# Kernel optimization log

Hardware: AMD Instinct MI355X
Metric: run time of the kernel (lower is better)

The kernel has to match this reference:

```python
import jax, jax.numpy as jnp
import numpy as np

HEADS = 8
DIM_HEAD = 64
RMS_EPS = 1.1920929e-07  # torch default eps = finfo(fp32).eps


def rotate_half(x):
    x1, x2 = jnp.split(x, 2, axis=-1)
    return jnp.concatenate((-x2, x1), axis=-1)


def setup_inputs() -> dict:
    key = jax.random.key(0)
    k1, k2, k3, k4, k5 = jax.random.split(key, 5)
    b, n, dim = 2, 4096, 1024
    dim_hidden = HEADS * DIM_HEAD  # 512
    x = jax.random.normal(k1, (b, n, dim), dtype=jnp.float32)
    rotary_emb = jax.random.normal(k2, (n, DIM_HEAD), dtype=jnp.float32)
    rms_weight = jnp.ones((dim,), dtype=jnp.float32)
    w_qkv = jax.random.normal(k3, (dim, dim_hidden * 3), dtype=jnp.float32) * (dim ** -0.5)
    w_out = jax.random.normal(k4, (dim_hidden, dim), dtype=jnp.float32) * (dim_hidden ** -0.5)
    return {"x": x, "rotary_emb": rotary_emb, "rms_weight": rms_weight,
            "w_qkv": w_qkv, "w_out": w_out}


def reference(x, rotary_emb, rms_weight, w_qkv, w_out):
    b, n, dim = x.shape
    h, d = HEADS, DIM_HEAD
    # RMSNorm
    xn = x * jax.lax.rsqrt(jnp.mean(x * x, axis=-1, keepdims=True) + RMS_EPS) * rms_weight
    # QKV projection, rearrange 'b n (qkv h d) -> qkv b h n d'
    qkv = (xn @ w_qkv).reshape(b, n, 3, h, d).transpose(2, 0, 3, 1, 4)
    q, k, v = qkv[0], qkv[1], qkv[2]
    # RoPE
    cos, sin = jnp.cos(rotary_emb), jnp.sin(rotary_emb)  # (n, d) broadcasts over b,h
    q = q * cos + rotate_half(q) * sin
    k = k * cos + rotate_half(k) * sin
    q = q * (d ** -0.5)
    sim = jnp.einsum('bhid,bhjd->bhij', q, k)
    causal_mask = jnp.triu(jnp.ones((n, n), dtype=bool), 1)
    sim = jnp.where(causal_mask, -jnp.finfo(sim.dtype).max, sim)
    attn = jax.nn.softmax(sim, axis=-1)
    out = jnp.einsum('bhij,bhjd->bhid', attn, v)
    out = out.transpose(0, 2, 1, 3).reshape(b, n, h * d)  # 'b h n d -> b n (h d)'
    return out @ w_out
```

## Files before the change

### kernel.cpp

```cpp
#include <hip/hip_runtime.h>
#include <hip/hip_bf16.h>
#include <cstdint>

using bf16x8 = __attribute__((ext_vector_type(8))) __bf16;
using f32x4  = __attribute__((ext_vector_type(4))) float;

#define LOG2E 1.4426950408889634f

__device__ inline void gload16(__bf16* lds, const __bf16* g) {
    __builtin_amdgcn_global_load_lds((const __attribute__((address_space(1))) void*)g,
                                     (__attribute__((address_space(3))) void*)lds, 16, 0, 0);
}
__device__ inline void wait_barrier4() {
    asm volatile("s_waitcnt vmcnt(4)" ::: "memory");
    __builtin_amdgcn_s_barrier();
}
__device__ inline void wait_barrier0() {
    asm volatile("s_waitcnt vmcnt(0)" ::: "memory");
    __builtin_amdgcn_s_barrier();
}

__global__ __launch_bounds__(256) void rmsnorm_kernel(const float* __restrict__ x,
                                                      const float* __restrict__ w,
                                                      __bf16* __restrict__ xn) {
    const int row = blockIdx.x;
    const float4 v = reinterpret_cast<const float4*>(x + (size_t)row * 1024)[threadIdx.x];
    float ss = v.x * v.x + v.y * v.y + v.z * v.z + v.w * v.w;
#pragma unroll
    for (int i = 1; i < 64; i <<= 1) ss += __shfl_xor(ss, i);
    __shared__ float part[4];
    if ((threadIdx.x & 63) == 0) part[threadIdx.x >> 6] = ss;
    __syncthreads();
    const float total = part[0] + part[1] + part[2] + part[3];
    const float scale = rsqrtf(total * (1.0f / 1024.0f) + 1.1920929e-07f);
    const float4 wv = reinterpret_cast<const float4*>(w)[threadIdx.x];
    union { __bf16 h[4]; uint2 u; } pk;
    pk.h[0] = (__bf16)(v.x * scale * wv.x);
    pk.h[1] = (__bf16)(v.y * scale * wv.y);
    pk.h[2] = (__bf16)(v.z * scale * wv.z);
    pk.h[3] = (__bf16)(v.w * scale * wv.w);
    reinterpret_cast<uint2*>(xn + (size_t)row * 1024)[threadIdx.x] = pk.u;
}

__global__ void transpose_cast_kernel(const float* __restrict__ in,
                                      __bf16* __restrict__ out, int K, int N) {
    __shared__ float tile[32][33];
    const int n0 = blockIdx.x * 32, k0 = blockIdx.y * 32;
#pragma unroll
    for (int r = threadIdx.y; r < 32; r += 8)
        tile[r][threadIdx.x] = in[(size_t)(k0 + r) * N + n0 + threadIdx.x];
    __syncthreads();
#pragma unroll
    for (int r = threadIdx.y; r < 32; r += 8)
        out[(size_t)(n0 + r) * K + k0 + threadIdx.x] = (__bf16)tile[threadIdx.x][r];
}

__global__ __launch_bounds__(256) void csin_kernel(const float* __restrict__ rot,
                                                   float2* __restrict__ csin) {
    const int i = blockIdx.x * 256 + threadIdx.x;
    float s, c;
    sincosf(rot[i], &s, &c);
    csin[i] = make_float2(c, s);
}

__global__ __launch_bounds__(256) void rope_kernel(__bf16* __restrict__ qk,
                                                   const float2* __restrict__ csin) {
    const int row = blockIdx.x * 4 + (threadIdx.x >> 6);
    const int lane = threadIdx.x & 63;
    const int h = lane >> 3, dl = (lane & 7) * 4;
    const int pos = row & 4095;
    const float4 csA = *reinterpret_cast<const float4*>(&csin[pos * 64 + dl]);
    const float4 csB = *reinterpret_cast<const float4*>(&csin[pos * 64 + dl + 2]);
    const float4 csC = *reinterpret_cast<const float4*>(&csin[pos * 64 + dl + 32]);
    const float4 csD = *reinterpret_cast<const float4*>(&csin[pos * 64 + dl + 34]);
    const float c0[4] = {csA.x, csA.z, csB.x, csB.z};
    const float s0[4] = {csA.y, csA.w, csB.y, csB.w};
    const float c1[4] = {csC.x, csC.z, csD.x, csD.z};
    const float s1[4] = {csC.y, csC.w, csD.y, csD.w};
    __bf16* p = qk + (size_t)row * 1024 + h * 64 + dl;
    const float qs = 0.125f * LOG2E;
#pragma unroll
    for (int part = 0; part < 2; ++part) {
        __bf16* pp = p + part * 512;
        const float sc = part ? 1.0f : qs;
        union { uint2 u; __bf16 hh[4]; } va, vb, oa, ob;
        va.u = *reinterpret_cast<const uint2*>(pp);
        vb.u = *reinterpret_cast<const uint2*>(pp + 32);
#pragma unroll
        for (int j = 0; j < 4; ++j) {
            const float a = (float)va.hh[j], b2 = (float)vb.hh[j];
            oa.hh[j] = (__bf16)((a * c0[j] - b2 * s0[j]) * sc);
            ob.hh[j] = (__bf16)((b2 * c1[j] + a * s1[j]) * sc);
        }
        *reinterpret_cast<uint2*>(pp)      = oa.u;
        *reinterpret_cast<uint2*>(pp + 32) = ob.u;
    }
}

template <typename OutT, int MODE>
__global__ __launch_bounds__(256) void gemm_bt(const __bf16* __restrict__ A,
                                               const __bf16* __restrict__ Bt,
                                               OutT* __restrict__ C,
                                               __bf16* __restrict__ vt,
                                               int M, int N, int K) {
    __shared__ __align__(16) __bf16 As[3][128 * 32];
    __shared__ __align__(16) __bf16 Bs[3][128 * 32];
    const int bm = blockIdx.y, bn = blockIdx.x;
    const int tid = threadIdx.x;
    const int w = tid >> 6, l = tid & 63, lg = l >> 4, lr = l & 15;
    const int wr = w >> 1, wc = w & 1;
    const __bf16* Ab = A + (size_t)(bm * 128) * K;
    const __bf16* Bb = Bt + (size_t)(bn * 128) * K;
    const int srow = tid >> 2, scol = (tid & 3) * 8;
    const __bf16* Asrc = Ab + (size_t)srow * K + scol;
    const __bf16* Bsrc = Bb + (size_t)srow * K + scol;

    auto stage = [&](int k2) {
        const int nx = k2 % 3;
        const int off = k2 * 32;
        gload16(&As[nx][tid * 8],        Asrc + off);
        gload16(&As[nx][2048 + tid * 8], Asrc + (size_t)64 * K + off);
        gload16(&Bs[nx][tid * 8],        Bsrc + off);
        gload16(&Bs[nx][2048 + tid * 8], Bsrc + (size_t)64 * K + off);
    };

    const int NS = K >> 5;
    f32x4 acc[4][4] = {};
    stage(0);
    stage(1);
    wait_barrier4();
    for (int k = 0; k < NS; ++k) {
        const bool more = (k + 2 < NS);
        if (more) stage(k + 2);
        const __bf16* Ac = &As[k % 3][0];
        const __bf16* Bc = &Bs[k % 3][0];
        bf16x8 af[4], bfr[4];
#pragma unroll
        for (int m = 0; m < 4; ++m)
            af[m] = *reinterpret_cast<const bf16x8*>(Ac + (wr * 64 + m * 16 + lr) * 32 + lg * 8);
#pragma unroll
        for (int nn = 0; nn < 4; ++nn)
            bfr[nn] = *reinterpret_cast<const bf16x8*>(Bc + (wc * 64 + nn * 16 + lr) * 32 + lg * 8);
#pragma unroll
        for (int m = 0; m < 4; ++m)
#pragma unroll
            for (int nn = 0; nn < 4; ++nn)
                acc[m][nn] = __builtin_amdgcn_mfma_f32_16x16x32_bf16(af[m], bfr[nn],
                                                                     acc[m][nn], 0, 0, 0);
        if (more) wait_barrier4();
        else      wait_barrier0();
    }
    if constexpr (MODE == 1) {
        const int cb = bn * 128 + wc * 64;
        if (cb < 1024) {
#pragma unroll
            for (int m = 0; m < 4; ++m) {
                const int rg = bm * 128 + wr * 64 + m * 16 + 4 * lg;
#pragma unroll
                for (int nn = 0; nn < 4; ++nn) {
                    const int cg = cb + nn * 16 + lr;
#pragma unroll
                    for (int r = 0; r < 4; ++r)
                        C[(size_t)(rg + r) * 1024 + cg] = (OutT)acc[m][nn][r];
                }
            }
        } else {
#pragma unroll
            for (int m = 0; m < 4; ++m) {
                const int rg = bm * 128 + wr * 64 + m * 16 + 4 * lg;
                const int bidx = rg >> 12, pos0 = rg & 4095;
                const int a0 = pos0 & 63;
                const int cp = 32 * (a0 >> 5) + 8 * ((a0 >> 2) & 3) + 4 * ((a0 >> 4) & 1);
                const int nbase = (pos0 & ~63) + cp;
#pragma unroll
                for (int nn = 0; nn < 4; ++nn) {
                    const int col = cb + nn * 16 + lr - 1024;
                    const int hh = col >> 6, dd = col & 63;
                    union { __bf16 h4[4]; uint2 u; } pk2;
#pragma unroll
                    for (int r = 0; r < 4; ++r) pk2.h4[r] = (__bf16)acc[m][nn][r];
                    *reinterpret_cast<uint2*>(&vt[((size_t)(bidx * 8 + hh) * 64 + dd) * 4096 + nbase]) = pk2.u;
                }
            }
        }
        return;
    }
#pragma unroll
    for (int m = 0; m < 4; ++m) {
        const int rg = bm * 128 + wr * 64 + m * 16 + 4 * lg;
#pragma unroll
        for (int nn = 0; nn < 4; ++nn) {
            const int cg = bn * 128 + wc * 64 + nn * 16 + lr;
#pragma unroll
            for (int r = 0; r < 4; ++r)
                C[(size_t)(rg + r) * N + cg] = (OutT)acc[m][nn][r];
        }
    }
}

__global__ __launch_bounds__(256) void attn_kernel(const __bf16* __restrict__ qkp,
                                                   const __bf16* __restrict__ vt,
                                                   __bf16* __restrict__ attn_out) {
    const int bid = blockIdx.x;
    const int swz = (bid & 7) * 64 + (bid >> 3);
    const int bh  = swz >> 5;
    const int p   = swz & 31;
    const int b = bh >> 3, h = bh & 7;
    const int tid = threadIdx.x;
    const int w = tid >> 6, l = tid & 63, lg = l >> 4, lr = l & 15;

    __shared__ __align__(16) __bf16 Ks[4][64 * 64];
    __shared__ __align__(16) __bf16 Vs[4][64 * 64];

    const __bf16* qbase = qkp + (size_t)b * 4096 * 1024 + h * 64;
    const __bf16* kbase = qbase + 512;
    const __bf16* vtb   = vt + (size_t)(b * 8 + h) * 64 * 4096;

    const int sr = tid >> 3;
    const int sc = ((tid & 7) ^ (sr & 7)) * 8;
    const __bf16* ksrc0 = kbase + (size_t)sr * 1024 + sc;
    const __bf16* vsrc0 = vtb + (size_t)sr * 4096 + sc;

    const int xel = (lr & 7) * 8;

    for (int seg = 0; seg < 2; ++seg) {
        const int qt = seg ? (63 - p) : p;
        const int wq0 = qt * 64 + 16 * w;
        const int nkt = qt + 1;

        bf16x8 Qf[2];
#pragma unroll
        for (int kh = 0; kh < 2; ++kh)
            Qf[kh] = *reinterpret_cast<const bf16x8*>(
                qbase + (size_t)(wq0 + lr) * 1024 + 32 * kh + 8 * lg);

        f32x4 O[4] = {};
        float m_ = -1e30f, l_ = 0.0f;
        const __bf16* kp = ksrc0;
        const __bf16* vp = vsrc0;

        auto stage2 = [&](__bf16* kdst, __bf16* vdst) {
            gload16(kdst + tid * 8,         kp);
            gload16(kdst + (tid + 256) * 8, kp + 32 * 1024);
            gload16(vdst + tid * 8,         vp);
            gload16(vdst + (tid + 256) * 8, vp + 32 * 4096);
            kp += 64 * 1024;
            vp += 64;
        };
        auto qk_step = [&](f32x4 (&S)[4], const __bf16* kb) {
            __builtin_amdgcn_s_setprio(1);
#pragma unroll
            for (int jt = 0; jt < 4; ++jt) {
                const __bf16* kr = kb + (16 * jt + lr) * 64;
                const bf16x8 Kf0 = *reinterpret_cast<const bf16x8*>(kr + ((8 * lg) ^ xel));
                const bf16x8 Kf1 = *reinterpret_cast<const bf16x8*>(kr + ((32 + 8 * lg) ^ xel));
                f32x4 z = {};
                z = __builtin_amdgcn_mfma_f32_16x16x32_bf16(Kf0, Qf[0], z, 0, 0, 0);
                S[jt] = __builtin_amdgcn_mfma_f32_16x16x32_bf16(Kf1, Qf[1], z, 0, 0, 0);
            }
            __builtin_amdgcn_s_setprio(0);
        };
        auto smpv = [&](f32x4 (&SC)[4], const __bf16* vb, bool domask) {
            if (domask) {
#pragma unroll
                for (int jt = 0; jt < 4; ++jt)
#pragma unroll
                    for (int r = 0; r < 4; ++r)
                        if (16 * jt + 4 * lg + r > 16 * w + lr) SC[jt][r] = -1e30f;
            }
            float mx = -1e30f;
#pragma unroll
            for (int jt = 0; jt < 4; ++jt)
                mx = fmaxf(mx, fmaxf(fmaxf(SC[jt][0], SC[jt][1]), fmaxf(SC[jt][2], SC[jt][3])));
            if (__any(mx > m_ + 8.0f)) {
                mx = fmaxf(mx, __shfl_xor(mx, 16));
                mx = fmaxf(mx, __shfl_xor(mx, 32));
                const float mn = fmaxf(m_, mx);
                const float alpha = __builtin_amdgcn_exp2f(m_ - mn);
                m_ = mn;
                l_ *= alpha;
#pragma unroll
                for (int dt = 0; dt < 4; ++dt) O[dt] *= alpha;
            }
            float sum = 0.0f;
#pragma unroll
            for (int jt = 0; jt < 4; ++jt)
#pragma unroll
                for (int r = 0; r < 4; ++r) {
                    const float pv = __builtin_amdgcn_exp2f(SC[jt][r] - m_);
                    SC[jt][r] = pv;
                    sum += pv;
                }
            l_ += sum;
            __builtin_amdgcn_s_setprio(1);
#pragma unroll
            for (int s = 0; s < 2; ++s) {
                bf16x8 Pf;
#pragma unroll
                for (int i = 0; i < 8; ++i)
                    Pf[i] = (__bf16)SC[2 * s + (i >> 2)][i & 3];
#pragma unroll
                for (int dt = 0; dt < 4; ++dt) {
                    const bf16x8 Vf = *reinterpret_cast<const bf16x8*>(
                        vb + (16 * dt + lr) * 64 + ((32 * s + 8 * lg) ^ xel));
                    O[dt] = __builtin_amdgcn_mfma_f32_16x16x32_bf16(Vf, Pf, O[dt], 0, 0, 0);
                }
            }
            __builtin_amdgcn_s_setprio(0);
        };

        f32x4 S0[4], S1[4];
        int t = 0;

        stage2(Ks[0], Vs[0]);
        stage2(Ks[1], Vs[1]);
        stage2(Ks[2], Vs[2]);
        wait_barrier4();
        qk_step(S0, Ks[0]);

        for (; t + 8 <= nkt; t += 4) {
            stage2(Ks[3], Vs[3]); qk_step(S1, Ks[1]); smpv(S0, Vs[0], false); wait_barrier4();
            stage2(Ks[0], Vs[0]); qk_step(S0, Ks[2]); smpv(S1, Vs[1], false); wait_barrier4();
            stage2(Ks[1], Vs[1]); qk_step(S1, Ks[3]); smpv(S0, Vs[2], false); wait_barrier4();
            stage2(Ks[2], Vs[2]); qk_step(S0, Ks[0]); smpv(S1, Vs[3], false); wait_barrier4();
        }

        {
            f32x4 Sp[4];
#pragma unroll
            for (int jt = 0; jt < 4; ++jt) Sp[jt] = S0[jt];
            for (; t < nkt; ++t) {
                const bool more3 = (t + 3 < nkt);
                if (more3) stage2(Ks[(t + 3) & 3], Vs[(t + 3) & 3]);
                f32x4 Sn[4];
                if (t + 1 < nkt) qk_step(Sn, Ks[(t + 1) & 3]);
                smpv(Sp, Vs[t & 3], t == nkt - 1);
                if (more3) wait_barrier4();
                else       wait_barrier0();
#pragma unroll
                for (int jt = 0; jt < 4; ++jt) Sp[jt] = Sn[jt];
            }
        }

        float lt = l_;
        lt += __shfl_xor(lt, 16);
        lt += __shfl_xor(lt, 32);
        const float inv = 1.0f / lt;
        __bf16* op = attn_out + ((size_t)b * 4096 + wq0 + lr) * 512 + h * 64;
#pragma unroll
        for (int dt = 0; dt < 4; ++dt) {
            union { __bf16 h4[4]; uint2 u; } ow;
#pragma unroll
            for (int r = 0; r < 4; ++r) ow.h4[r] = (__bf16)(O[dt][r] * inv);
            *reinterpret_cast<uint2*>(op + 16 * dt + 4 * lg) = ow.u;
        }
    }
}

extern "C" void kernel_launch(void* const* d_in, const int* in_sizes, int n_in,
                              void* d_out, int out_size, void* d_ws, size_t ws_size,
                              hipStream_t stream) {
    (void)in_sizes; (void)n_in; (void)out_size; (void)ws_size;
    const float* x    = (const float*)d_in[0];
    const float* rot  = (const float*)d_in[1];
    const float* rmsw = (const float*)d_in[2];
    const float* wqkv = (const float*)d_in[3];
    const float* wout = (const float*)d_in[4];
    float* out = (float*)d_out;

    char* ws = (char*)d_ws;
    __bf16* xn    = (__bf16*)ws;
    __bf16* wqkvt = (__bf16*)(ws + 16777216);
    __bf16* woutt = (__bf16*)(ws + 16777216 + 3145728);
    __bf16* aout  = (__bf16*)(ws + 16777216 + 3145728 + 1048576);
    __bf16* qk   = (__bf16*)d_out;
    float2* csin = (float2*)((char*)d_out + 16777216);
    __bf16* vt   = (__bf16*)((char*)d_out + 18874368);

    rmsnorm_kernel<<<8192, 256, 0, stream>>>(x, rmsw, xn);
    transpose_cast_kernel<<<dim3(48, 32), dim3(32, 8), 0, stream>>>(wqkv, wqkvt, 1024, 1536);
    transpose_cast_kernel<<<dim3(32, 16), dim3(32, 8), 0, stream>>>(wout, woutt, 512, 1024);
    csin_kernel<<<1024, 256, 0, stream>>>(rot, csin);
    gemm_bt<__bf16, 1><<<dim3(12, 64), 256, 0, stream>>>(xn, wqkvt, qk, vt, 8192, 1536, 1024);
    rope_kernel<<<2048, 256, 0, stream>>>(qk, csin);
    attn_kernel<<<512, 256, 0, stream>>>(qk, vt, aout);
    gemm_bt<float, 0><<<dim3(8, 64), 256, 0, stream>>>(aout, woutt, out, nullptr, 8192, 1024, 512);
}
```

Measured before the change: 142.8 us.

## Split attention into one query tile per block, triple-buffer KV, stage GEMM epilogue via LDS

The attention kernel now launches 1024 blocks, each handling a single query tile. Tiles are ordered longest-first so the causal workload balances across CUs. This replaces the old scheme where each of 512 blocks processed a paired short and long tile. The KV ring buffer shrinks from 4 to 3 stages, which cuts LDS use so more blocks can be resident, but the waits become full __syncthreads drains instead of partial vmcnt waits. Separately, the GEMM epilogue stages accumulators through LDS so each row is written with wide coalesced 16-byte stores rather than scattered scalar stores.

```diff
diff --git a/kernel.cpp b/kernel.cpp
--- a/kernel.cpp
+++ b/kernel.cpp
@@ -150,21 +150,10 @@
         if (more) wait_barrier4();
         else      wait_barrier0();
     }
+
+    const int cb = bn * 128 + wc * 64;
     if constexpr (MODE == 1) {
-        const int cb = bn * 128 + wc * 64;
-        if (cb < 1024) {
-#pragma unroll
-            for (int m = 0; m < 4; ++m) {
-                const int rg = bm * 128 + wr * 64 + m * 16 + 4 * lg;
-#pragma unroll
-                for (int nn = 0; nn < 4; ++nn) {
-                    const int cg = cb + nn * 16 + lr;
-#pragma unroll
-                    for (int r = 0; r < 4; ++r)
-                        C[(size_t)(rg + r) * 1024 + cg] = (OutT)acc[m][nn][r];
-                }
-            }
-        } else {
+        if (cb >= 1024) {
 #pragma unroll
             for (int m = 0; m < 4; ++m) {
                 const int rg = bm * 128 + wr * 64 + m * 16 + 4 * lg;
@@ -182,18 +171,36 @@
                     *reinterpret_cast<uint2*>(&vt[((size_t)(bidx * 8 + hh) * 64 + dd) * 4096 + nbase]) = pk2.u;
                 }
             }
-        }
-        return;
-    }
+            return;
+        }
+    }
+    float* tb = reinterpret_cast<float*>(&As[0][0]) + w * 1088;
+    const int row = l >> 2, c4 = (l & 3) * 16;
 #pragma unroll
     for (int m = 0; m < 4; ++m) {
-        const int rg = bm * 128 + wr * 64 + m * 16 + 4 * lg;
-#pragma unroll
-        for (int nn = 0; nn < 4; ++nn) {
-            const int cg = bn * 128 + wc * 64 + nn * 16 + lr;
+#pragma unroll
+        for (int nn = 0; nn < 4; ++nn)
 #pragma unroll
             for (int r = 0; r < 4; ++r)
-                C[(size_t)(rg + r) * N + cg] = (OutT)acc[m][nn][r];
+                tb[(4 * lg + r) * 68 + nn * 16 + lr] = acc[m][nn][r];
+        const int rg2 = bm * 128 + wr * 64 + m * 16 + row;
+        float v[16];
+#pragma unroll
+        for (int j = 0; j < 4; ++j)
+            *reinterpret_cast<float4*>(v + 4 * j) =
+                *reinterpret_cast<const float4*>(tb + row * 68 + c4 + 4 * j);
+        if constexpr (MODE == 1) {
+            union { __bf16 h16[16]; uint4 u4[2]; } ob;
+#pragma unroll
+            for (int j = 0; j < 16; ++j) ob.h16[j] = (__bf16)v[j];
+            uint4* dst = reinterpret_cast<uint4*>(C + (size_t)rg2 * 1024 + cb + c4);
+            dst[0] = ob.u4[0];
+            dst[1] = ob.u4[1];
+        } else {
+#pragma unroll
+            for (int j = 0; j < 4; ++j)
+                *reinterpret_cast<float4*>(&C[(size_t)rg2 * N + cb + c4 + 4 * j]) =
+                    *reinterpret_cast<const float4*>(v + 4 * j);
         }
     }
 }
@@ -202,15 +209,15 @@
                                                    const __bf16* __restrict__ vt,
                                                    __bf16* __restrict__ attn_out) {
     const int bid = blockIdx.x;
-    const int swz = (bid & 7) * 64 + (bid >> 3);
-    const int bh  = swz >> 5;
-    const int p   = swz & 31;
+    const int j = bid >> 3;
+    const int bh = 2 * (bid & 7) + (j & 1);
+    const int qt = 63 - (j >> 1);
     const int b = bh >> 3, h = bh & 7;
     const int tid = threadIdx.x;
     const int w = tid >> 6, l = tid & 63, lg = l >> 4, lr = l & 15;
 
-    __shared__ __align__(16) __bf16 Ks[4][64 * 64];
-    __shared__ __align__(16) __bf16 Vs[4][64 * 64];
+    __shared__ __align__(16) __bf16 Ks[3][64 * 64];
+    __shared__ __align__(16) __bf16 Vs[3][64 * 64];
 
     const __bf16* qbase = qkp + (size_t)b * 4096 * 1024 + h * 64;
     const __bf16* kbase = qbase + 512;
@@ -218,142 +225,136 @@
 
     const int sr = tid >> 3;
     const int sc = ((tid & 7) ^ (sr & 7)) * 8;
-    const __bf16* ksrc0 = kbase + (size_t)sr * 1024 + sc;
-    const __bf16* vsrc0 = vtb + (size_t)sr * 4096 + sc;
+    const __bf16* kp = kbase + (size_t)sr * 1024 + sc;
+    const __bf16* vp = vtb + (size_t)sr * 4096 + sc;
 
     const int xel = (lr & 7) * 8;
 
-    for (int seg = 0; seg < 2; ++seg) {
-        const int qt = seg ? (63 - p) : p;
-        const int wq0 = qt * 64 + 16 * w;
-        const int nkt = qt + 1;
-
-        bf16x8 Qf[2];
-#pragma unroll
-        for (int kh = 0; kh < 2; ++kh)
-            Qf[kh] = *reinterpret_cast<const bf16x8*>(
-                qbase + (size_t)(wq0 + lr) * 1024 + 32 * kh + 8 * lg);
-
-        f32x4 O[4] = {};
-        float m_ = -1e30f, l_ = 0.0f;
-        const __bf16* kp = ksrc0;
-        const __bf16* vp = vsrc0;
-
-        auto stage2 = [&](__bf16* kdst, __bf16* vdst) {
-            gload16(kdst + tid * 8,         kp);
-            gload16(kdst + (tid + 256) * 8, kp + 32 * 1024);
-            gload16(vdst + tid * 8,         vp);
-            gload16(vdst + (tid + 256) * 8, vp + 32 * 4096);
-            kp += 64 * 1024;
-            vp += 64;
-        };
-        auto qk_step = [&](f32x4 (&S)[4], const __bf16* kb) {
-            __builtin_amdgcn_s_setprio(1);
-#pragma unroll
-            for (int jt = 0; jt < 4; ++jt) {
-                const __bf16* kr = kb + (16 * jt + lr) * 64;
-                const bf16x8 Kf0 = *reinterpret_cast<const bf16x8*>(kr + ((8 * lg) ^ xel));
-                const bf16x8 Kf1 = *reinterpret_cast<const bf16x8*>(kr + ((32 + 8 * lg) ^ xel));
-                f32x4 z = {};
-                z = __builtin_amdgcn_mfma_f32_16x16x32_bf16(Kf0, Qf[0], z, 0, 0, 0);
-                S[jt] = __builtin_amdgcn_mfma_f32_16x16x32_bf16(Kf1, Qf[1], z, 0, 0, 0);
+    const int wq0 = qt * 64 + 16 * w;
+    const int nkt = qt + 1;
+
+    bf16x8 Qf[2];
+#pragma unroll
+    for (int kh = 0; kh < 2; ++kh)
+        Qf[kh] = *reinterpret_cast<const bf16x8*>(
+            qbase + (size_t)(wq0 + lr) * 1024 + 32 * kh + 8 * lg);
+
+    f32x4 O[4] = {};
+    float m_ = -1e30f, l_ = 0.0f;
+
+    auto stage2 = [&](__bf16* kdst, __bf16* vdst) {
+        gload16(kdst + tid * 8,         kp);
+        gload16(kdst + (tid + 256) * 8, kp + 32 * 1024);
+        gload16(vdst + tid * 8,         vp);
+        gload16(vdst + (tid + 256) * 8, vp + 32 * 4096);
+        kp += 64 * 1024;
+        vp += 64;
+    };
+    auto qk_step = [&](f32x4 (&S)[4], const __bf16* kb) {
+        __builtin_amdgcn_s_setprio(1);
+#pragma unroll
+        for (int jt = 0; jt < 4; ++jt) {
+            const __bf16* kr = kb + (16 * jt + lr) * 64;
+            const bf16x8 Kf0 = *reinterpret_cast<const bf16x8*>(kr + ((8 * lg) ^ xel));
+            const bf16x8 Kf1 = *reinterpret_cast<const bf16x8*>(kr + ((32 + 8 * lg) ^ xel));
+            f32x4 z = {};
+            z = __builtin_amdgcn_mfma_f32_16x16x32_bf16(Kf0, Qf[0], z, 0, 0, 0);
+            S[jt] = __builtin_amdgcn_mfma_f32_16x16x32_bf16(Kf1, Qf[1], z, 0, 0, 0);
+        }
+        __builtin_amdgcn_s_setprio(0);
+    };
+    auto smpv = [&](f32x4 (&SC)[4], const __bf16* vb, bool domask) {
+        if (domask) {
+#pragma unroll
+            for (int jt = 0; jt < 4; ++jt)
+#pragma unroll
+                for (int r = 0; r < 4; ++r)
+                    if (16 * jt + 4 * lg + r > 16 * w + lr) SC[jt][r] = -1e30f;
+        }
+        float mx = -1e30f;
+#pragma unroll
+        for (int jt = 0; jt < 4; ++jt)
+            mx = fmaxf(mx, fmaxf(fmaxf(SC[jt][0], SC[jt][1]), fmaxf(SC[jt][2], SC[jt][3])));
+        if (__any(mx > m_ + 8.0f)) {
+            mx = fmaxf(mx, __shfl_xor(mx, 16));
+            mx = fmaxf(mx, __shfl_xor(mx, 32));
+            const float mn = fmaxf(m_, mx);
+            const float alpha = __builtin_amdgcn_exp2f(m_ - mn);
+            m_ = mn;
+            l_ *= alpha;
+#pragma unroll
+            for (int dt = 0; dt < 4; ++dt) O[dt] *= alpha;
+        }
+        float sum = 0.0f;
+#pragma unroll
+        for (int jt = 0; jt < 4; ++jt)
+#pragma unroll
+            for (int r = 0; r < 4; ++r) {
+                const float pv = __builtin_amdgcn_exp2f(SC[jt][r] - m_);
+                SC[jt][r] = pv;
+                sum += pv;
             }
-            __builtin_amdgcn_s_setprio(0);
-        };
-        auto smpv = [&](f32x4 (&SC)[4], const __bf16* vb, bool domask) {
-            if (domask) {
-#pragma unroll
-                for (int jt = 0; jt < 4; ++jt)
-#pragma unroll
-                    for (int r = 0; r < 4; ++r)
-                        if (16 * jt + 4 * lg + r > 16 * w + lr) SC[jt][r] = -1e30f;
+        l_ += sum;
+        __builtin_amdgcn_s_setprio(1);
+#pragma unroll
+        for (int s = 0; s < 2; ++s) {
+            bf16x8 Pf;
+#pragma unroll
+            for (int i = 0; i < 8; ++i)
+                Pf[i] = (__bf16)SC[2 * s + (i >> 2)][i & 3];
+#pragma unroll
+            for (int dt = 0; dt < 4; ++dt) {
+                const bf16x8 Vf = *reinterpret_cast<const bf16x8*>(
+                    vb + (16 * dt + lr) * 64 + ((32 * s + 8 * lg) ^ xel));
+                O[dt] = __builtin_amdgcn_mfma_f32_16x16x32_bf16(Vf, Pf, O[dt], 0, 0, 0);
             }
-            float mx = -1e30f;
-#pragma unroll
-            for (int jt = 0; jt < 4; ++jt)
-                mx = fmaxf(mx, fmaxf(fmaxf(SC[jt][0], SC[jt][1]), fmaxf(SC[jt][2], SC[jt][3])));
-            if (__any(mx > m_ + 8.0f)) {
-                mx = fmaxf(mx, __shfl_xor(mx, 16));
-                mx = fmaxf(mx, __shfl_xor(mx, 32));
-                const float mn = fmaxf(m_, mx);
-                const float alpha = __builtin_amdgcn_exp2f(m_ - mn);
-                m_ = mn;
-                l_ *= alpha;
-#pragma unroll
-                for (int dt = 0; dt < 4; ++dt) O[dt] *= alpha;
-            }
-            float sum = 0.0f;
-#pragma unroll
-            for (int jt = 0; jt < 4; ++jt)
-#pragma unroll
-                for (int r = 0; r < 4; ++r) {
-                    const float pv = __builtin_amdgcn_exp2f(SC[jt][r] - m_);
-                    SC[jt][r] = pv;
-                    sum += pv;
-                }
-            l_ += sum;
-            __builtin_amdgcn_s_setprio(1);
-#pragma unroll
-            for (int s = 0; s < 2; ++s) {
-                bf16x8 Pf;
-#pragma unroll
-                for (int i = 0; i < 8; ++i)
-                    Pf[i] = (__bf16)SC[2 * s + (i >> 2)][i & 3];
-#pragma unroll
-                for (int dt = 0; dt < 4; ++dt) {
-                    const bf16x8 Vf = *reinterpret_cast<const bf16x8*>(
-                        vb + (16 * dt + lr) * 64 + ((32 * s + 8 * lg) ^ xel));
-                    O[dt] = __builtin_amdgcn_mfma_f32_16x16x32_bf16(Vf, Pf, O[dt], 0, 0, 0);
-                }
-            }
-            __builtin_amdgcn_s_setprio(0);
-        };
-
-        f32x4 S0[4], S1[4];
-        int t = 0;
-
-        stage2(Ks[0], Vs[0]);
-        stage2(Ks[1], Vs[1]);
-        stage2(Ks[2], Vs[2]);
-        wait_barrier4();
-        qk_step(S0, Ks[0]);
-
-        for (; t + 8 <= nkt; t += 4) {
-            stage2(Ks[3], Vs[3]); qk_step(S1, Ks[1]); smpv(S0, Vs[0], false); wait_barrier4();
-            stage2(Ks[0], Vs[0]); qk_step(S0, Ks[2]); smpv(S1, Vs[1], false); wait_barrier4();
-            stage2(Ks[1], Vs[1]); qk_step(S1, Ks[3]); smpv(S0, Vs[2], false); wait_barrier4();
-            stage2(Ks[2], Vs[2]); qk_step(S0, Ks[0]); smpv(S1, Vs[3], false); wait_barrier4();
-        }
-
-        {
-            f32x4 Sp[4];
-#pragma unroll
-            for (int jt = 0; jt < 4; ++jt) Sp[jt] = S0[jt];
-            for (; t < nkt; ++t) {
-                const bool more3 = (t + 3 < nkt);
-                if (more3) stage2(Ks[(t + 3) & 3], Vs[(t + 3) & 3]);
-                f32x4 Sn[4];
-                if (t + 1 < nkt) qk_step(Sn, Ks[(t + 1) & 3]);
-                smpv(Sp, Vs[t & 3], t == nkt - 1);
-                if (more3) wait_barrier4();
-                else       wait_barrier0();
-#pragma unroll
-                for (int jt = 0; jt < 4; ++jt) Sp[jt] = Sn[jt];
-            }
-        }
-
-        float lt = l_;
-        lt += __shfl_xor(lt, 16);
-        lt += __shfl_xor(lt, 32);
-        const float inv = 1.0f / lt;
-        __bf16* op = attn_out + ((size_t)b * 4096 + wq0 + lr) * 512 + h * 64;
-#pragma unroll
-        for (int dt = 0; dt < 4; ++dt) {
-            union { __bf16 h4[4]; uint2 u; } ow;
-#pragma unroll
-            for (int r = 0; r < 4; ++r) ow.h4[r] = (__bf16)(O[dt][r] * inv);
-            *reinterpret_cast<uint2*>(op + 16 * dt + 4 * lg) = ow.u;
-        }
+        }
+        __builtin_amdgcn_s_setprio(0);
+    };
+
+    f32x4 S0[4], S1[4];
+    int t = 0;
+
+    stage2(Ks[0], Vs[0]);
+    stage2(Ks[1], Vs[1]);
+    __syncthreads();
+    qk_step(S0, Ks[0]);
+
+    for (; t + 8 <= nkt; t += 6) {
+        stage2(Ks[2], Vs[2]); qk_step(S1, Ks[1]); smpv(S0, Vs[0], false); __syncthreads();
+        stage2(Ks[0], Vs[0]); qk_step(S0, Ks[2]); smpv(S1, Vs[1], false); __syncthreads();
+        stage2(Ks[1], Vs[1]); qk_step(S1, Ks[0]); smpv(S0, Vs[2], false); __syncthreads();
+        stage2(Ks[2], Vs[2]); qk_step(S0, Ks[1]); smpv(S1, Vs[0], false); __syncthreads();
+        stage2(Ks[0], Vs[0]); qk_step(S1, Ks[2]); smpv(S0, Vs[1], false); __syncthreads();
+        stage2(Ks[1], Vs[1]); qk_step(S0, Ks[0]); smpv(S1, Vs[2], false); __syncthreads();
+    }
+
+    {
+        f32x4 Sp[4];
+#pragma unroll
+        for (int jt = 0; jt < 4; ++jt) Sp[jt] = S0[jt];
+        for (; t < nkt; ++t) {
+            if (t + 2 < nkt) stage2(Ks[(t + 2) % 3], Vs[(t + 2) % 3]);
+            f32x4 Sn[4];
+            if (t + 1 < nkt) qk_step(Sn, Ks[(t + 1) % 3]);
+            smpv(Sp, Vs[t % 3], t == nkt - 1);
+            __syncthreads();
+#pragma unroll
+            for (int jt = 0; jt < 4; ++jt) Sp[jt] = Sn[jt];
+        }
+    }
+
+    float lt = l_;
+    lt += __shfl_xor(lt, 16);
+    lt += __shfl_xor(lt, 32);
+    const float inv = 1.0f / lt;
+    __bf16* op = attn_out + ((size_t)b * 4096 + wq0 + lr) * 512 + h * 64;
+#pragma unroll
+    for (int dt = 0; dt < 4; ++dt) {
+        union { __bf16 h4[4]; uint2 u; } ow;
+#pragma unroll
+        for (int r = 0; r < 4; ++r) ow.h4[r] = (__bf16)(O[dt][r] * inv);
+        *reinterpret_cast<uint2*>(op + 16 * dt + 4 * lg) = ow.u;
     }
 }
 
@@ -383,6 +384,6 @@
     csin_kernel<<<1024, 256, 0, stream>>>(rot, csin);
     gemm_bt<__bf16, 1><<<dim3(12, 64), 256, 0, stream>>>(xn, wqkvt, qk, vt, 8192, 1536, 1024);
     rope_kernel<<<2048, 256, 0, stream>>>(qk, csin);
-    attn_kernel<<<512, 256, 0, stream>>>(qk, vt, aout);
+    attn_kernel<<<1024, 256, 0, stream>>>(qk, vt, aout);
     gemm_bt<float, 0><<<dim3(8, 64), 256, 0, stream>>>(aout, woutt, out, nullptr, 8192, 1024, 512);
 }
```

After: 145.8 us. 2.1% more time.
